# Optimization experiments

Hardware: AMD Instinct MI355X
Metric: run time of the kernel (lower is better)

Reference implementation:

```python
import jax, jax.numpy as jnp
import numpy as np

N_NODES, N_EDGES, N_GRAPHS = 200000, 600000, 4000
IN_DIM, EDGE_DIM, HIDDEN, DEPTH = 25, 11, 128, 4
BN_EPS = 1e-5

def lrelu(x):
    return jnp.where(x > 0, x, 0.1 * x)

def setup_inputs() -> dict:
    key = jax.random.key(0)
    ks = jax.random.split(key, 8)
    x = jax.random.normal(ks[0], (N_NODES, IN_DIM), jnp.float32)
    edge_index = jax.random.randint(ks[1], (2, N_EDGES), 0, N_NODES, jnp.int32)
    edge_attr = jax.random.normal(ks[2], (N_EDGES, EDGE_DIM), jnp.float32)
    batch = jnp.sort(jax.random.randint(ks[3], (N_NODES,), 0, N_GRAPHS, jnp.int32))
    def init_w(k, shape, fan_in):
        return jax.random.normal(k, shape, jnp.float32) * np.float32(1.0 / np.sqrt(fan_in))
    W_in = init_w(ks[4], (IN_DIM, HIDDEN), IN_DIM)
    b_in = jnp.zeros((HIDDEN,), jnp.float32)
    W_msg = init_w(ks[5], (DEPTH, HIDDEN + EDGE_DIM, HIDDEN), HIDDEN + EDGE_DIM)
    b_msg = jnp.zeros((DEPTH, HIDDEN), jnp.float32)
    W_up = init_w(ks[6], (DEPTH, 2 * HIDDEN, HIDDEN), 2 * HIDDEN)
    b_up = jnp.zeros((DEPTH, HIDDEN), jnp.float32)
    gamma = jnp.ones((DEPTH, HIDDEN), jnp.float32)
    beta = jnp.zeros((DEPTH, HIDDEN), jnp.float32)
    return dict(x=x, edge_index=edge_index, edge_attr=edge_attr, batch=batch,
                W_in=W_in, b_in=b_in, W_msg=W_msg, b_msg=b_msg,
                W_up=W_up, b_up=b_up, gamma=gamma, beta=beta)

def reference(x, edge_index, edge_attr, batch, W_in, b_in, W_msg, b_msg, W_up, b_up, gamma, beta):
    N = x.shape[0]
    src, dst = edge_index[0], edge_index[1]  # PyG: x_j = x[src], aggregate at dst
    h = lrelu(x @ W_in + b_in)  # input_proj + leaky_relu(0.1)
    depth = W_msg.shape[0]
    for i in range(depth):
        # message: leaky_relu(Linear(cat[x_j, edge_attr]))
        msg = lrelu(jnp.concatenate([h[src], edge_attr], axis=-1) @ W_msg[i] + b_msg[i])
        aggr = jax.ops.segment_sum(msg, dst, num_segments=N)  # scatter-add
        # update: leaky_relu(Linear(cat[aggr, x]))
        out = lrelu(jnp.concatenate([aggr, h], axis=-1) @ W_up[i] + b_up[i])
        out = jax.nn.relu(out)
        # BatchNorm over node dim (training-mode batch statistics)
        mu = out.mean(axis=0)
        var = out.var(axis=0)
        h = gamma[i] * (out - mu) * jax.lax.rsqrt(var + BN_EPS) + beta[i]
        # dropout is identity at eval
    cnt = jax.ops.segment_sum(jnp.ones((N,), h.dtype), batch, num_segments=N_GRAPHS)
    summed = jax.ops.segment_sum(h, batch, num_segments=N_GRAPHS)
    return summed / jnp.maximum(cnt, 1.0)[:, None]  # global_mean_pool -> [G, H]
```

## Files before the change

kernel.cpp:

```cpp
#include <hip/hip_runtime.h>

#define N_NODES  200000
#define N_EDGES  600000
#define N_GRAPHS 4000
#define IN_DIM   25
#define EDGE_DIM 11
#define HIDDEN   128
#define DEPTH    4
#define BN_EPS   1e-5f

#define UB   32
#define NBLK (N_NODES / UB)
#define NEBLK (N_EDGES / 64)
#define CHUNK  256
#define NCHUNK ((N_NODES + CHUNK - 1) / CHUNK)

typedef unsigned short ushortT;
typedef __attribute__((ext_vector_type(8))) short short8v;
typedef __attribute__((ext_vector_type(4))) float float4v;

__device__ __forceinline__ float lrelu(float v) { return v > 0.f ? v : 0.1f * v; }

__device__ __forceinline__ ushortT f2bf(float f) {
    unsigned u = __builtin_bit_cast(unsigned, f);
    u = (u + 0x7fffu + ((u >> 16) & 1u)) >> 16;
    return (ushortT)u;
}
__device__ __forceinline__ float bf2f(ushortT h) {
    unsigned u = ((unsigned)h) << 16;
    return __builtin_bit_cast(float, u);
}

__global__ void k_hist(const int* __restrict__ ei, int* __restrict__ cnt)
{
    const int e = blockIdx.x * 256 + threadIdx.x;
    if (e < N_EDGES) atomicAdd(&cnt[ei[N_EDGES + e]], 1);
}

__global__ __launch_bounds__(256) void k_chunk_sum(const int* __restrict__ cnt,
                                                   int* __restrict__ bsum)
{
    const int t = threadIdx.x;
    const int i = blockIdx.x * CHUNK + t;
    int v = (i < N_NODES) ? cnt[i] : 0;
    #pragma unroll
    for (int off = 32; off > 0; off >>= 1) v += __shfl_down(v, off);
    __shared__ int ws[4];
    if ((t & 63) == 0) ws[t >> 6] = v;
    __syncthreads();
    if (t == 0) bsum[blockIdx.x] = ws[0] + ws[1] + ws[2] + ws[3];
}

__global__ __launch_bounds__(1024) void k_scan_bsums(const int* __restrict__ bsum,
                                                     int* __restrict__ bscan)
{
    __shared__ int s[1024];
    const int t = threadIdx.x;
    const int v = (t < NCHUNK) ? bsum[t] : 0;
    s[t] = v; __syncthreads();
    for (int off = 1; off < 1024; off <<= 1) {
        const int x = (t >= off) ? s[t - off] : 0;
        __syncthreads();
        s[t] += x;
        __syncthreads();
    }
    if (t < NCHUNK) bscan[t] = s[t] - v;
}

__global__ __launch_bounds__(256) void k_chunk_scan(const int* __restrict__ cnt,
                                                    const int* __restrict__ bscan,
                                                    int* __restrict__ off_work)
{
    __shared__ int s[CHUNK];
    const int b = blockIdx.x, t = threadIdx.x;
    const int i = b * CHUNK + t;
    const int v = (i < N_NODES) ? cnt[i] : 0;
    s[t] = v; __syncthreads();
    for (int off = 1; off < CHUNK; off <<= 1) {
        const int x = (t >= off) ? s[t - off] : 0;
        __syncthreads();
        s[t] += x;
        __syncthreads();
    }
    if (i < N_NODES) off_work[i] = bscan[b] + s[t] - v;
}

__global__ void k_scatter(const int* __restrict__ ei, int* __restrict__ off_work,
                          int* __restrict__ srcS, int* __restrict__ dstS,
                          int* __restrict__ perm)
{
    const int e = blockIdx.x * 256 + threadIdx.x;
    if (e < N_EDGES) {
        const int d = ei[N_EDGES + e];
        const int pos = atomicAdd(&off_work[d], 1);
        srcS[pos] = ei[e];
        dstS[pos] = d;
        perm[pos] = e;
    }
}

__global__ void k_flag_ends(const int* __restrict__ dstS, int* __restrict__ flag)
{
    const int i = blockIdx.x * 256 + threadIdx.x;
    if (i < NEBLK * 4) {
        const int b = i >> 2, p = i & 3;
        const int pos = (p == 0) ? 0 : (p == 1) ? 31 : (p == 2) ? 32 : 63;
        flag[dstS[b * 64 + pos]] = 1;
    }
}

__global__ void k_flag_zdeg(const int* __restrict__ ecnt, int* __restrict__ flag)
{
    const int n = blockIdx.x * 256 + threadIdx.x;
    if (n < N_NODES && ecnt[n] == 0) flag[n] = 1;
}

__global__ void k_compact(const int* __restrict__ flag, int* __restrict__ zlist,
                          int* __restrict__ zcount)
{
    const int n = blockIdx.x * 256 + threadIdx.x;
    if (n < N_NODES && flag[n]) zlist[atomicAdd(zcount, 1)] = n;
}

__global__ __launch_bounds__(256) void k_zero_rows(const int* __restrict__ zlist,
                                                   const int* __restrict__ zcount,
                                                   float* __restrict__ aggr)
{
    const int total = zcount[0] * 32;
    const float4 z = {0.f, 0.f, 0.f, 0.f};
    for (int i = blockIdx.x * 256 + threadIdx.x; i < total; i += gridDim.x * 256) {
        const int row = zlist[i >> 5], q = i & 31;
        reinterpret_cast<float4*>(aggr)[(size_t)row * 32 + q] = z;
    }
}

__global__ __launch_bounds__(256) void k_prep_ea(const float* __restrict__ ea,
                                                 const int* __restrict__ perm,
                                                 ushortT* __restrict__ ea16)
{
    const size_t i = (size_t)blockIdx.x * 256 + threadIdx.x;
    if (i >= (size_t)N_EDGES * 16) return;
    const int e = (int)(i >> 4), c = (int)(i & 15);
    const int pe = perm[e];
    ea16[i] = (c < EDGE_DIM) ? f2bf(ea[(size_t)pe * EDGE_DIM + c]) : (ushortT)0;
}

__global__ __launch_bounds__(256) void k_fold(const float* __restrict__ Wm,
                                              const float* __restrict__ bm,
                                              const float* __restrict__ Wu,
                                              const float* __restrict__ bu,
                                              const float* __restrict__ scale,
                                              const float* __restrict__ shift,
                                              ushortT* __restrict__ WmF,
                                              float*   __restrict__ bmF,
                                              ushortT* __restrict__ WuF,
                                              float*   __restrict__ buF)
{
    const int b = blockIdx.x, t = threadIdx.x;
    if (b < 80) {
        const int i = b * 256 + t;
        const int j = i & 7, lane = (i >> 3) & 63, tile = i >> 9;
        const int ct = tile & 7, kt = tile >> 3;
        const int k = kt * 32 + ((lane >> 4) << 3) + j;
        const int c = ct * 16 + (lane & 15);
        float v = (k < HIDDEN + EDGE_DIM) ? Wm[k * HIDDEN + c] : 0.f;
        if (k < HIDDEN) v *= scale[k];
        WmF[i] = f2bf(v);
    } else if (b < 208) {
        const int i = (b - 80) * 256 + t;
        const int j = i & 7, lane = (i >> 3) & 63, tile = i >> 9;
        const int ct = tile & 7, kt = tile >> 3;
        const int k = kt * 32 + ((lane >> 4) << 3) + j;
        const int c = ct * 16 + (lane & 15);
        float v = Wu[k * HIDDEN + c];
        if (k >= HIDDEN) v *= scale[k - HIDDEN];
        WuF[i] = f2bf(v);
    } else if (b == 208) {
        if (t < HIDDEN) {
            float acc = bm[t];
            for (int k = 0; k < HIDDEN; ++k) acc += shift[k] * Wm[k * HIDDEN + t];
            bmF[t] = acc;
        }
    } else {
        if (t < HIDDEN) {
            float acc = bu[t];
            for (int k = 0; k < HIDDEN; ++k) acc += shift[k] * Wu[(HIDDEN + k) * HIDDEN + t];
            buF[t] = acc;
        }
    }
}

__global__ void k_init_affine(float* __restrict__ scale, float* __restrict__ shift)
{
    const int t = threadIdx.x;
    scale[t] = 1.f;
    shift[t] = 0.f;
}

__global__ __launch_bounds__(128) void k_input_proj(const float* __restrict__ x,
                                                    const float* __restrict__ W,
                                                    const float* __restrict__ b,
                                                    ushortT* __restrict__ h16)
{
    const int t  = threadIdx.x;
    const int n0 = blockIdx.x * 8;
    __shared__ float sW[IN_DIM * HIDDEN];
    __shared__ float sx[8][IN_DIM];
    for (int i = t; i < IN_DIM * HIDDEN; i += 128) sW[i] = W[i];
    for (int i = t; i < 8 * IN_DIM; i += 128) {
        int n = i / IN_DIM, k = i % IN_DIM;
        sx[n][k] = x[(size_t)(n0 + n) * IN_DIM + k];
    }
    __syncthreads();
    const float bt = b[t];
    for (int n = 0; n < 8; ++n) {
        float acc = bt;
        #pragma unroll
        for (int k = 0; k < IN_DIM; ++k) acc += sx[n][k] * sW[k * HIDDEN + t];
        h16[(size_t)(n0 + n) * HIDDEN + t] = f2bf(lrelu(acc));
    }
}

__global__ __launch_bounds__(256) void k_edge_mfma(const ushortT* __restrict__ h16,
                                                   const int*     __restrict__ srcS,
                                                   const int*     __restrict__ dstS,
                                                   const ushortT* __restrict__ ea16,
                                                   const ushortT* __restrict__ Wf,
                                                   const float*   __restrict__ bmsg,
                                                   float*         __restrict__ aggr)
{
    const int t    = threadIdx.x;
    const int wave = t >> 6, lane = t & 63;
    const int e0   = blockIdx.x * 64;

    __shared__ __align__(16) unsigned char smem[64 * 132 * 4];
    ushortT (*sA)[168]   = reinterpret_cast<ushortT (*)[168]>(smem);
    float   (*sMsg)[132] = reinterpret_cast<float (*)[132]>(smem);
    __shared__ int sSrc[64];
    __shared__ int sDst[64];

    const int ct0 = wave * 2;
    short8v B[5][2];
    const short8v* wp = reinterpret_cast<const short8v*>(Wf);
    #pragma unroll
    for (int kt = 0; kt < 5; ++kt) {
        B[kt][0] = wp[(size_t)(kt * 8 + ct0) * 64 + lane];
        B[kt][1] = wp[(size_t)(kt * 8 + ct0 + 1) * 64 + lane];
    }

    if (t < 64) { sSrc[t] = srcS[e0 + t]; sDst[t] = dstS[e0 + t]; }
    __syncthreads();

    for (int i = t; i < 64 * 16; i += 256) {
        const int e = i >> 4, q = i & 15;
        const uint4 v = reinterpret_cast<const uint4*>(h16)[(size_t)sSrc[e] * 16 + q];
        *reinterpret_cast<uint4*>(&sA[e][q * 8]) = v;
    }
    for (int i = t; i < 64 * 2; i += 256) {
        const int e = i >> 1, q = i & 1;
        const uint4 v = reinterpret_cast<const uint4*>(ea16)[((size_t)(e0 + e)) * 2 + q];
        *reinterpret_cast<uint4*>(&sA[e][128 + q * 8]) = v;
    }
    if (t < 128) {
        const int e = t >> 1, q = t & 1;
        const uint4 z = {0u, 0u, 0u, 0u};
        *reinterpret_cast<uint4*>(&sA[e][144 + q * 8]) = z;
    }
    __syncthreads();

    float4v acc[4][2];
    #pragma unroll
    for (int m = 0; m < 4; ++m) { acc[m][0] = (float4v)(0.f); acc[m][1] = (float4v)(0.f); }

    const int kOff = (lane >> 4) * 8;
    #pragma unroll
    for (int m = 0; m < 4; ++m) {
        const int row = m * 16 + (lane & 15);
        #pragma unroll
        for (int kt = 0; kt < 5; ++kt) {
            const short8v a = *reinterpret_cast<const short8v*>(&sA[row][kt * 32 + kOff]);
            acc[m][0] = __builtin_amdgcn_mfma_f32_16x16x32_bf16(a, B[kt][0], acc[m][0], 0, 0, 0);
            acc[m][1] = __builtin_amdgcn_mfma_f32_16x16x32_bf16(a, B[kt][1], acc[m][1], 0, 0, 0);
        }
    }
    __syncthreads();

    const int col = lane & 15;
    const int r0  = (lane >> 4) * 4;
    #pragma unroll
    for (int c = 0; c < 2; ++c) {
        const int ccol = (ct0 + c) * 16 + col;
        const float bt = bmsg[ccol];
        #pragma unroll
        for (int m = 0; m < 4; ++m) {
            #pragma unroll
            for (int j = 0; j < 4; ++j) {
                sMsg[m * 16 + r0 + j][ccol] = lrelu(acc[m][c][j] + bt);
            }
        }
    }
    __syncthreads();

    const int half = t >> 7;
    const int c    = t & 127;
    const int base = half * 32;
    float a = 0.f;
    int cur = sDst[base];
    bool atStart = true;
    for (int e = base; e < base + 32; ++e) {
        const int d = sDst[e];
        if (d != cur) {
            if (atStart) atomicAdd(&aggr[(size_t)cur * HIDDEN + c], a);
            else         aggr[(size_t)cur * HIDDEN + c] = a;
            atStart = false; cur = d; a = 0.f;
        }
        a += sMsg[e][c];
    }
    atomicAdd(&aggr[(size_t)cur * HIDDEN + c], a);
}

__global__ __launch_bounds__(256) void k_update_mfma(const float*   __restrict__ aggr,
                                                     const ushortT* __restrict__ h16,
                                                     const ushortT* __restrict__ Wf,
                                                     const float*   __restrict__ bup,
                                                     ushortT*       __restrict__ hout,
                                                     float*         __restrict__ p_sum,
                                                     float*         __restrict__ p_sumsq)
{
    const int t    = threadIdx.x;
    const int wave = t >> 6, lane = t & 63;
    const int n0   = blockIdx.x * UB;

    __shared__ __align__(16) ushortT sA[UB][264];
    __shared__ __align__(16) ushortT sLo[UB][136];

    const int ct0 = wave * 2;
    short8v Bh[8][2];
    const short8v* wp = reinterpret_cast<const short8v*>(Wf);
    #pragma unroll
    for (int kt = 0; kt < 8; ++kt) {
        Bh[kt][0] = wp[(size_t)(kt * 8 + ct0) * 64 + lane];
        Bh[kt][1] = wp[(size_t)(kt * 8 + ct0 + 1) * 64 + lane];
    }

    for (int i = t; i < UB * 32; i += 256) {
        const int n = i >> 5, q = i & 31;
        const float4 v = reinterpret_cast<const float4*>(aggr)[(size_t)(n0 + n) * 32 + q];
        union { ushortT s[4]; uint2 u; } hi, lo;
        #pragma unroll
        for (int j = 0; j < 4; ++j) {
            const float f = (&v.x)[j];
            const ushortT hb = f2bf(f);
            hi.s[j] = hb;
            lo.s[j] = f2bf(f - bf2f(hb));
        }
        *reinterpret_cast<uint2*>(&sA[n][q * 4])  = hi.u;
        *reinterpret_cast<uint2*>(&sLo[n][q * 4]) = lo.u;
    }
    for (int i = t; i < UB * 16; i += 256) {
        const int n = i >> 4, q = i & 15;
        const uint4 v = reinterpret_cast<const uint4*>(h16)[(size_t)(n0 + n) * 16 + q];
        *reinterpret_cast<uint4*>(&sA[n][128 + q * 8]) = v;
    }
    __syncthreads();

    float4v acc[2][2];
    #pragma unroll
    for (int m = 0; m < 2; ++m) { acc[m][0] = (float4v)(0.f); acc[m][1] = (float4v)(0.f); }

    const int kOff = (lane >> 4) * 8;
    #pragma unroll
    for (int m = 0; m < 2; ++m) {
        const int row = m * 16 + (lane & 15);
        #pragma unroll
        for (int kt = 0; kt < 8; ++kt) {
            const short8v a = *reinterpret_cast<const short8v*>(&sA[row][kt * 32 + kOff]);
            acc[m][0] = __builtin_amdgcn_mfma_f32_16x16x32_bf16(a, Bh[kt][0], acc[m][0], 0, 0, 0);
            acc[m][1] = __builtin_amdgcn_mfma_f32_16x16x32_bf16(a, Bh[kt][1], acc[m][1], 0, 0, 0);
        }
        #pragma unroll
        for (int kt = 0; kt < 4; ++kt) {
            const short8v a = *reinterpret_cast<const short8v*>(&sLo[row][kt * 32 + kOff]);
            acc[m][0] = __builtin_amdgcn_mfma_f32_16x16x32_bf16(a, Bh[kt][0], acc[m][0], 0, 0, 0);
            acc[m][1] = __builtin_amdgcn_mfma_f32_16x16x32_bf16(a, Bh[kt][1], acc[m][1], 0, 0, 0);
        }
    }

    const int col = lane & 15;
    const int r0  = (lane >> 4) * 4;
    #pragma unroll
    for (int c = 0; c < 2; ++c) {
        const int ccol = (ct0 + c) * 16 + col;
        const float bt = bup[ccol];
        float s = 0.f, q = 0.f;
        #pragma unroll
        for (int m = 0; m < 2; ++m) {
            #pragma unroll
            for (int j = 0; j < 4; ++j) {
                const float v = fmaxf(acc[m][c][j] + bt, 0.f);
                s += v; q += v * v;
                hout[(size_t)(n0 + m * 16 + r0 + j) * HIDDEN + ccol] = f2bf(v);
            }
        }
        s += __shfl_xor(s, 16); s += __shfl_xor(s, 32);
        q += __shfl_xor(q, 16); q += __shfl_xor(q, 32);
        if (lane < 16) {
            p_sum  [(size_t)ccol * NBLK + blockIdx.x] = s;
            p_sumsq[(size_t)ccol * NBLK + blockIdx.x] = q;
        }
    }
}

__global__ __launch_bounds__(256) void k_bn_reduce(const float* __restrict__ p_sum,
                                                   const float* __restrict__ p_sumsq,
                                                   const float* __restrict__ gamma,
                                                   const float* __restrict__ beta,
                                                   float* __restrict__ scale,
                                                   float* __restrict__ shift)
{
    const int c = blockIdx.x, t = threadIdx.x;
    float s = 0.f, q = 0.f;
    for (int i = t; i < NBLK; i += 256) {
        s += p_sum  [(size_t)c * NBLK + i];
        q += p_sumsq[(size_t)c * NBLK + i];
    }
    #pragma unroll
    for (int off = 32; off > 0; off >>= 1) {
        s += __shfl_down(s, off);
        q += __shfl_down(q, off);
    }
    __shared__ float ls[4], lq[4];
    const int w = t >> 6;
    if ((t & 63) == 0) { ls[w] = s; lq[w] = q; }
    __syncthreads();
    if (t == 0) {
        s = ls[0] + ls[1] + ls[2] + ls[3];
        q = lq[0] + lq[1] + lq[2] + lq[3];
        const float mu  = s * (1.f / N_NODES);
        const float var = q * (1.f / N_NODES) - mu * mu;
        const float sc  = gamma[c] * rsqrtf(var + BN_EPS);
        scale[c] = sc;
        shift[c] = beta[c] - mu * sc;
    }
}

__global__ void k_pool_cnt(const int* __restrict__ batch, float* __restrict__ cnt)
{
    const int n = blockIdx.x * 256 + threadIdx.x;
    if (n < N_NODES) atomicAdd(&cnt[batch[n]], 1.0f);
}

__global__ __launch_bounds__(128) void k_pool_sum(const ushortT* __restrict__ h16,
                                                  const int* __restrict__ batch,
                                                  const float* __restrict__ scale,
                                                  const float* __restrict__ shift,
                                                  float* __restrict__ pool)
{
    const int t  = threadIdx.x;
    const int n0 = blockIdx.x * 16;
    __shared__ int sb[16];
    if (t < 16) sb[t] = batch[n0 + t];
    __syncthreads();
    const float sc = scale[t], sh = shift[t];
    int g = sb[0];
    float acc = 0.f;
    for (int j = 0; j < 16; ++j) {
        const float v = sc * bf2f(h16[(size_t)(n0 + j) * HIDDEN + t]) + sh;
        if (sb[j] != g) {
            atomicAdd(&pool[(size_t)g * HIDDEN + t], acc);
            g = sb[j];
            acc = v;
        } else {
            acc += v;
        }
    }
    atomicAdd(&pool[(size_t)g * HIDDEN + t], acc);
}

__global__ void k_pool_div(const float* __restrict__ pool,
                           const float* __restrict__ cnt,
                           float* __restrict__ out)
{
    const int i = blockIdx.x * 256 + threadIdx.x;
    if (i < N_GRAPHS * HIDDEN) {
        const int g = i >> 7;
        out[i] = pool[i] / fmaxf(cnt[g], 1.0f);
    }
}

extern "C" void kernel_launch(void* const* d_in, const int* in_sizes, int n_in,
                              void* d_out, int out_size, void* d_ws, size_t ws_size,
                              hipStream_t stream)
{
    const float* x     = (const float*)d_in[0];
    const int*   ei    = (const int*)  d_in[1];
    const float* ea    = (const float*)d_in[2];
    const int*   batch = (const int*)  d_in[3];
    const float* W_in  = (const float*)d_in[4];
    const float* b_in  = (const float*)d_in[5];
    const float* W_msg = (const float*)d_in[6];
    const float* b_msg = (const float*)d_in[7];
    const float* W_up  = (const float*)d_in[8];
    const float* b_up  = (const float*)d_in[9];
    const float* gamma = (const float*)d_in[10];
    const float* beta  = (const float*)d_in[11];
    float* out = (float*)d_out;

    float*   aggr  = (float*)d_ws;
    ushortT* hA    = (ushortT*)(aggr + (size_t)N_NODES * HIDDEN);
    ushortT* hB    = hA + (size_t)N_NODES * HIDDEN;
    ushortT* ea16  = hB + (size_t)N_NODES * HIDDEN;
    ushortT* wmsgfA = ea16 + (size_t)N_EDGES * 16;
    ushortT* wupfA  = wmsgfA + 20480;
    float*   biasM  = (float*)(wupfA + 32768);
    float*   biasU  = biasM + HIDDEN;
    float*   bn_scale = biasU + HIDDEN;
    float*   bn_shift = bn_scale + HIDDEN;
    float*   pool     = bn_shift + HIDDEN;
    float*   cnt      = pool + (size_t)N_GRAPHS * HIDDEN;
    float*   p_sum    = cnt + N_GRAPHS;
    float*   p_sumsq  = p_sum + (size_t)HIDDEN * NBLK;
    int*     ecnt     = (int*)(p_sumsq + (size_t)HIDDEN * NBLK);
    int*     off_work = ecnt + N_NODES;
    int*     bsum     = off_work + N_NODES;
    int*     bscan    = bsum + 1024;
    int*     srcS     = bscan + 1024;
    int*     dstS     = srcS + N_EDGES;
    int*     perm     = dstS + N_EDGES;
    int*     flag     = perm + N_EDGES;
    int*     zlist    = flag + N_NODES;
    int*     zcount   = zlist + N_NODES;

    hipMemsetAsync(ecnt, 0, N_NODES * sizeof(int), stream);
    hipMemsetAsync(flag, 0, N_NODES * sizeof(int), stream);
    hipMemsetAsync(zcount, 0, sizeof(int), stream);
    k_hist<<<(N_EDGES + 255) / 256, 256, 0, stream>>>(ei, ecnt);
    k_chunk_sum<<<NCHUNK, 256, 0, stream>>>(ecnt, bsum);
    k_scan_bsums<<<1, 1024, 0, stream>>>(bsum, bscan);
    k_chunk_scan<<<NCHUNK, 256, 0, stream>>>(ecnt, bscan, off_work);
    k_scatter<<<(N_EDGES + 255) / 256, 256, 0, stream>>>(ei, off_work, srcS, dstS, perm);
    k_flag_ends<<<(NEBLK * 4 + 255) / 256, 256, 0, stream>>>(dstS, flag);
    k_flag_zdeg<<<(N_NODES + 255) / 256, 256, 0, stream>>>(ecnt, flag);
    k_compact<<<(N_NODES + 255) / 256, 256, 0, stream>>>(flag, zlist, zcount);

    k_prep_ea<<<(N_EDGES * 16 + 255) / 256, 256, 0, stream>>>(ea, perm, ea16);
    k_input_proj<<<N_NODES / 8, 128, 0, stream>>>(x, W_in, b_in, hA);
    k_init_affine<<<1, 128, 0, stream>>>(bn_scale, bn_shift);

    ushortT* hcur = hA;
    ushortT* hnext = hB;
    for (int d = 0; d < DEPTH; ++d) {
        k_fold<<<210, 256, 0, stream>>>(
            W_msg + (size_t)d * (HIDDEN + EDGE_DIM) * HIDDEN, b_msg + (size_t)d * HIDDEN,
            W_up + (size_t)d * 2 * HIDDEN * HIDDEN, b_up + (size_t)d * HIDDEN,
            bn_scale, bn_shift, wmsgfA, biasM, wupfA, biasU);
        k_zero_rows<<<1024, 256, 0, stream>>>(zlist, zcount, aggr);
        k_edge_mfma<<<N_EDGES / 64, 256, 0, stream>>>(
            hcur, srcS, dstS, ea16, wmsgfA, biasM, aggr);
        k_update_mfma<<<N_NODES / UB, 256, 0, stream>>>(
            aggr, hcur, wupfA, biasU, hnext, p_sum, p_sumsq);
        k_bn_reduce<<<HIDDEN, 256, 0, stream>>>(p_sum, p_sumsq,
                                                gamma + (size_t)d * HIDDEN,
                                                beta + (size_t)d * HIDDEN,
                                                bn_scale, bn_shift);
        ushortT* tmp = hcur; hcur = hnext; hnext = tmp;
    }

    hipMemsetAsync(pool, 0, ((size_t)N_GRAPHS * HIDDEN + N_GRAPHS) * sizeof(float), stream);
    k_pool_cnt<<<(N_NODES + 255) / 256, 256, 0, stream>>>(batch, cnt);
    k_pool_sum<<<N_NODES / 16, 128, 0, stream>>>(hcur, batch, bn_scale, bn_shift, pool);
    k_pool_div<<<(N_GRAPHS * HIDDEN + 255) / 256, 256, 0, stream>>>(pool, cnt, out);
}
```

Before: 883.4 us.

## Shrink edge-kernel LDS with two-phase reduction and widen update kernel to 8 waves

The edge kernel now writes messages to shared memory in two 32-row phases, so its LDS footprint drops to the size of the A tile. Its segmented reduction runs over 16-edge runs, and the zero/flag bookkeeping is updated to match the new run boundaries. The update kernel moves to 512 threads, with each wave owning one 16-column tile, which halves per-thread registers and accumulators. The BN partial sums are stored node-block-major. The aim is higher occupancy in both hot kernels, at the cost of extra barriers and more direct-store/atomic boundaries per edge block.

After: 927.6 us. 5.0% more time.

```diff
diff --git a/kernel.cpp b/kernel.cpp
--- a/kernel.cpp
+++ b/kernel.cpp
@@ -102,10 +102,10 @@
 __global__ void k_flag_ends(const int* __restrict__ dstS, int* __restrict__ flag)
 {
     const int i = blockIdx.x * 256 + threadIdx.x;
-    if (i < NEBLK * 4) {
-        const int b = i >> 2, p = i & 3;
-        const int pos = (p == 0) ? 0 : (p == 1) ? 31 : (p == 2) ? 32 : 63;
-        flag[dstS[b * 64 + pos]] = 1;
+    if (i < NEBLK * 8) {
+        const int b = i >> 3, p = i & 7;
+        const int pp = (p >> 1) * 16 + ((p & 1) ? 15 : 0);
+        flag[dstS[b * 64 + pp]] = 1;
     }
 }
 
@@ -233,7 +233,7 @@
     const int wave = t >> 6, lane = t & 63;
     const int e0   = blockIdx.x * 64;
 
-    __shared__ __align__(16) unsigned char smem[64 * 132 * 4];
+    __shared__ __align__(16) unsigned char smem[64 * 168 * 2];
     ushortT (*sA)[168]   = reinterpret_cast<ushortT (*)[168]>(smem);
     float   (*sMsg)[132] = reinterpret_cast<float (*)[132]>(smem);
     __shared__ int sSrc[64];
@@ -287,39 +287,45 @@
 
     const int col = lane & 15;
     const int r0  = (lane >> 4) * 4;
-    #pragma unroll
-    for (int c = 0; c < 2; ++c) {
-        const int ccol = (ct0 + c) * 16 + col;
-        const float bt = bmsg[ccol];
-        #pragma unroll
-        for (int m = 0; m < 4; ++m) {
+    const int grp = t >> 7;
+    const int c   = t & 127;
+
+    #pragma unroll
+    for (int phase = 0; phase < 2; ++phase) {
+        #pragma unroll
+        for (int mm = 0; mm < 2; ++mm) {
+            const int m = phase * 2 + mm;
             #pragma unroll
-            for (int j = 0; j < 4; ++j) {
-                sMsg[m * 16 + r0 + j][ccol] = lrelu(acc[m][c][j] + bt);
+            for (int cc = 0; cc < 2; ++cc) {
+                const int ccol = (ct0 + cc) * 16 + col;
+                const float bt = bmsg[ccol];
+                #pragma unroll
+                for (int j = 0; j < 4; ++j) {
+                    sMsg[mm * 16 + r0 + j][ccol] = lrelu(acc[m][cc][j] + bt);
+                }
             }
         }
-    }
-    __syncthreads();
-
-    const int half = t >> 7;
-    const int c    = t & 127;
-    const int base = half * 32;
-    float a = 0.f;
-    int cur = sDst[base];
-    bool atStart = true;
-    for (int e = base; e < base + 32; ++e) {
-        const int d = sDst[e];
-        if (d != cur) {
-            if (atStart) atomicAdd(&aggr[(size_t)cur * HIDDEN + c], a);
-            else         aggr[(size_t)cur * HIDDEN + c] = a;
-            atStart = false; cur = d; a = 0.f;
-        }
-        a += sMsg[e][c];
-    }
-    atomicAdd(&aggr[(size_t)cur * HIDDEN + c], a);
-}
-
-__global__ __launch_bounds__(256) void k_update_mfma(const float*   __restrict__ aggr,
+        __syncthreads();
+        const int base = phase * 32 + grp * 16;
+        float a = 0.f;
+        int cur = sDst[base];
+        bool atStart = true;
+        for (int i = 0; i < 16; ++i) {
+            const int e = base + i;
+            const int d = sDst[e];
+            if (d != cur) {
+                if (atStart) atomicAdd(&aggr[(size_t)cur * HIDDEN + c], a);
+                else         aggr[(size_t)cur * HIDDEN + c] = a;
+                atStart = false; cur = d; a = 0.f;
+            }
+            a += sMsg[e - phase * 32][c];
+        }
+        atomicAdd(&aggr[(size_t)cur * HIDDEN + c], a);
+        __syncthreads();
+    }
+}
+
+__global__ __launch_bounds__(512) void k_update_mfma(const float*   __restrict__ aggr,
                                                      const ushortT* __restrict__ h16,
                                                      const ushortT* __restrict__ Wf,
                                                      const float*   __restrict__ bup,
@@ -334,16 +340,13 @@
     __shared__ __align__(16) ushortT sA[UB][264];
     __shared__ __align__(16) ushortT sLo[UB][136];
 
-    const int ct0 = wave * 2;
-    short8v Bh[8][2];
+    const int ct = wave;
+    short8v Bh[8];
     const short8v* wp = reinterpret_cast<const short8v*>(Wf);
     #pragma unroll
-    for (int kt = 0; kt < 8; ++kt) {
-        Bh[kt][0] = wp[(size_t)(kt * 8 + ct0) * 64 + lane];
-        Bh[kt][1] = wp[(size_t)(kt * 8 + ct0 + 1) * 64 + lane];
-    }
-
-    for (int i = t; i < UB * 32; i += 256) {
+    for (int kt = 0; kt < 8; ++kt) Bh[kt] = wp[(size_t)(kt * 8 + ct) * 64 + lane];
+
+    for (int i = t; i < UB * 32; i += 512) {
         const int n = i >> 5, q = i & 31;
         const float4 v = reinterpret_cast<const float4*>(aggr)[(size_t)(n0 + n) * 32 + q];
         union { ushortT s[4]; uint2 u; } hi, lo;
@@ -357,16 +360,15 @@
         *reinterpret_cast<uint2*>(&sA[n][q * 4])  = hi.u;
         *reinterpret_cast<uint2*>(&sLo[n][q * 4]) = lo.u;
     }
-    for (int i = t; i < UB * 16; i += 256) {
+    for (int i = t; i < UB * 16; i += 512) {
         const int n = i >> 4, q = i & 15;
         const uint4 v = reinterpret_cast<const uint4*>(h16)[(size_t)(n0 + n) * 16 + q];
         *reinterpret_cast<uint4*>(&sA[n][128 + q * 8]) = v;
     }
     __syncthreads();
 
-    float4v acc[2][2];
-    #pragma unroll
-    for (int m = 0; m < 2; ++m) { acc[m][0] = (float4v)(0.f); acc[m][1] = (float4v)(0.f); }
+    float4v acc[2];
+    acc[0] = (float4v)(0.f); acc[1] = (float4v)(0.f);
 
     const int kOff = (lane >> 4) * 8;
     #pragma unroll
@@ -375,39 +377,34 @@
         #pragma unroll
         for (int kt = 0; kt < 8; ++kt) {
             const short8v a = *reinterpret_cast<const short8v*>(&sA[row][kt * 32 + kOff]);
-            acc[m][0] = __builtin_amdgcn_mfma_f32_16x16x32_bf16(a, Bh[kt][0], acc[m][0], 0, 0, 0);
-            acc[m][1] = __builtin_amdgcn_mfma_f32_16x16x32_bf16(a, Bh[kt][1], acc[m][1], 0, 0, 0);
+            acc[m] = __builtin_amdgcn_mfma_f32_16x16x32_bf16(a, Bh[kt], acc[m], 0, 0, 0);
         }
         #pragma unroll
         for (int kt = 0; kt < 4; ++kt) {
             const short8v a = *reinterpret_cast<const short8v*>(&sLo[row][kt * 32 + kOff]);
-            acc[m][0] = __builtin_amdgcn_mfma_f32_16x16x32_bf16(a, Bh[kt][0], acc[m][0], 0, 0, 0);
-            acc[m][1] = __builtin_amdgcn_mfma_f32_16x16x32_bf16(a, Bh[kt][1], acc[m][1], 0, 0, 0);
-        }
-    }
-
-    const int col = lane & 15;
-    const int r0  = (lane >> 4) * 4;
-    #pragma unroll
-    for (int c = 0; c < 2; ++c) {
-        const int ccol = (ct0 + c) * 16 + col;
-        const float bt = bup[ccol];
-        float s = 0.f, q = 0.f;
-        #pragma unroll
-        for (int m = 0; m < 2; ++m) {
-            #pragma unroll
-            for (int j = 0; j < 4; ++j) {
-                const float v = fmaxf(acc[m][c][j] + bt, 0.f);
-                s += v; q += v * v;
-                hout[(size_t)(n0 + m * 16 + r0 + j) * HIDDEN + ccol] = f2bf(v);
-            }
-        }
-        s += __shfl_xor(s, 16); s += __shfl_xor(s, 32);
-        q += __shfl_xor(q, 16); q += __shfl_xor(q, 32);
-        if (lane < 16) {
-            p_sum  [(size_t)ccol * NBLK + blockIdx.x] = s;
-            p_sumsq[(size_t)ccol * NBLK + blockIdx.x] = q;
-        }
+            acc[m] = __builtin_amdgcn_mfma_f32_16x16x32_bf16(a, Bh[kt], acc[m], 0, 0, 0);
+        }
+    }
+
+    const int col  = lane & 15;
+    const int r0   = (lane >> 4) * 4;
+    const int ccol = ct * 16 + col;
+    const float bt = bup[ccol];
+    float s = 0.f, q = 0.f;
+    #pragma unroll
+    for (int m = 0; m < 2; ++m) {
+        #pragma unroll
+        for (int j = 0; j < 4; ++j) {
+            const float v = fmaxf(acc[m][j] + bt, 0.f);
+            s += v; q += v * v;
+            hout[(size_t)(n0 + m * 16 + r0 + j) * HIDDEN + ccol] = f2bf(v);
+        }
+    }
+    s += __shfl_xor(s, 16); s += __shfl_xor(s, 32);
+    q += __shfl_xor(q, 16); q += __shfl_xor(q, 32);
+    if (lane < 16) {
+        p_sum  [(size_t)blockIdx.x * HIDDEN + ccol] = s;
+        p_sumsq[(size_t)blockIdx.x * HIDDEN + ccol] = q;
     }
 }
 
@@ -421,8 +418,8 @@
     const int c = blockIdx.x, t = threadIdx.x;
     float s = 0.f, q = 0.f;
     for (int i = t; i < NBLK; i += 256) {
-        s += p_sum  [(size_t)c * NBLK + i];
-        q += p_sumsq[(size_t)c * NBLK + i];
+        s += p_sum  [(size_t)i * HIDDEN + c];
+        q += p_sumsq[(size_t)i * HIDDEN + c];
     }
     #pragma unroll
     for (int off = 32; off > 0; off >>= 1) {
@@ -539,7 +536,7 @@
     k_scan_bsums<<<1, 1024, 0, stream>>>(bsum, bscan);
     k_chunk_scan<<<NCHUNK, 256, 0, stream>>>(ecnt, bscan, off_work);
     k_scatter<<<(N_EDGES + 255) / 256, 256, 0, stream>>>(ei, off_work, srcS, dstS, perm);
-    k_flag_ends<<<(NEBLK * 4 + 255) / 256, 256, 0, stream>>>(dstS, flag);
+    k_flag_ends<<<(NEBLK * 8 + 255) / 256, 256, 0, stream>>>(dstS, flag);
     k_flag_zdeg<<<(N_NODES + 255) / 256, 256, 0, stream>>>(ecnt, flag);
     k_compact<<<(N_NODES + 255) / 256, 256, 0, stream>>>(flag, zlist, zcount);
 
@@ -557,7 +554,7 @@
         k_zero_rows<<<1024, 256, 0, stream>>>(zlist, zcount, aggr);
         k_edge_mfma<<<N_EDGES / 64, 256, 0, stream>>>(
             hcur, srcS, dstS, ea16, wmsgfA, biasM, aggr);
-        k_update_mfma<<<N_NODES / UB, 256, 0, stream>>>(
+        k_update_mfma<<<N_NODES / UB, 512, 0, stream>>>(
             aggr, hcur, wupfA, biasU, hnext, p_sum, p_sumsq);
         k_bn_reduce<<<HIDDEN, 256, 0, stream>>>(p_sum, p_sumsq,
                                                 gamma + (size_t)d * HIDDEN,
```
